# Performance work log

Hardware: AMD Instinct MI355X
Metric: run time of the kernel (lower is better)

The kernel has to match this reference:

```python
import jax, jax.numpy as jnp
import numpy as np

B, M, N = 4, 1024, 32768

def setup_inputs() -> dict:
    key = jax.random.key(0)
    k1, k2 = jax.random.split(key)
    keypoints = jax.random.normal(k1, (B, 3, M), dtype=jnp.float32)
    pc = jax.random.normal(k2, (B, 3, N), dtype=jnp.float32)
    return {"keypoints": keypoints, "pc": pc}

def reference(keypoints, pc):
    # Pairwise Euclidean distances via the expanded quadratic form:
    # ||k - p||^2 = ||k||^2 + ||p||^2 - 2 k.p  -> avoids the [B,3,M,N] tensor.
    k2 = jnp.sum(keypoints * keypoints, axis=1)            # [B, M]
    p2 = jnp.sum(pc * pc, axis=1)                          # [B, N]
    cross = jnp.einsum("bdm,bdn->bmn", keypoints, pc)     # [B, M, N]
    d2 = k2[:, :, None] + p2[:, None, :] - 2.0 * cross     # [B, M, N]
    dist = jnp.sqrt(jnp.maximum(d2, 0.0))
    min_dist = jnp.min(dist, axis=2)                       # [B, M]
    return jnp.mean(min_dist)
```

## Files before the change

### kernel.cpp

```cpp
#include <hip/hip_runtime.h>
#include <math.h>

#define BATCH 4
#define M 1024
#define NPTS 32768
#define NSPLIT 128
#define CHUNK (NPTS / NSPLIT)
#define KPT 4
#define TPB 256
#define RBLOCKS 16

#define Q_OFF      0
#define D2P_OFF    (2u << 20)
#define GSUM_OFF   (4u << 20)
#define CNT_OFF    ((4u << 20) + 4u)

__global__ __launch_bounds__(256) void p2p_prep(
        const float* __restrict__ pc, float4* __restrict__ q,
        float* __restrict__ gsum, unsigned* __restrict__ counter) {
    int i = blockIdx.x * 256 + threadIdx.x;
    int b = i >> 15;
    int n = i & (NPTS - 1);
    const float* p = pc + (size_t)b * 3 * NPTS;
    float x = p[n], y = p[NPTS + n], z = p[2 * NPTS + n];
    float hp = -0.5f * fmaf(x, x, fmaf(y, y, z * z));
    q[i] = make_float4(x, y, z, hp);
    if (i == 0) { *gsum = 0.f; *counter = 0u; }
}

__global__ __launch_bounds__(TPB) void p2p_main(
        const float* __restrict__ kp, const float4* __restrict__ q,
        float* __restrict__ d2p) {
    const int b = blockIdx.x / NSPLIT;
    const int c = blockIdx.x % NSPLIT;
    const int t = threadIdx.x;

    const float4* qc = q + b * NPTS + c * CHUNK;
    const float* kpb = kp + (size_t)b * 3 * M;

    float kx[KPT], ky[KPT], kz[KPT], k2[KPT], md[KPT];
#pragma unroll
    for (int k = 0; k < KPT; ++k) {
        int m = t + k * TPB;
        kx[k] = kpb[m];
        ky[k] = kpb[M + m];
        kz[k] = kpb[2 * M + m];
        k2[k] = fmaf(kx[k], kx[k], fmaf(ky[k], ky[k], kz[k] * kz[k]));
        md[k] = -INFINITY;
    }

#pragma unroll 2
    for (int j = 0; j < CHUNK; j += 4) {
        float4 q0 = qc[j + 0];
        float4 q1 = qc[j + 1];
        float4 q2 = qc[j + 2];
        float4 q3 = qc[j + 3];
#pragma unroll
        for (int k = 0; k < KPT; ++k) {
            float v0 = fmaf(kx[k], q0.x, fmaf(ky[k], q0.y, fmaf(kz[k], q0.z, q0.w)));
            float v1 = fmaf(kx[k], q1.x, fmaf(ky[k], q1.y, fmaf(kz[k], q1.z, q1.w)));
            float v2 = fmaf(kx[k], q2.x, fmaf(ky[k], q2.y, fmaf(kz[k], q2.z, q2.w)));
            float v3 = fmaf(kx[k], q3.x, fmaf(ky[k], q3.y, fmaf(kz[k], q3.z, q3.w)));
            md[k] = fmaxf(md[k], fmaxf(fmaxf(v0, v1), fmaxf(v2, v3)));
        }
    }

#pragma unroll
    for (int k = 0; k < KPT; ++k) {
        float d2 = fmaxf(fmaf(-2.f, md[k], k2[k]), 0.f);
        d2p[c * (BATCH * M) + b * M + t + k * TPB] = d2;
    }
}

__global__ __launch_bounds__(256) void p2p_reduce(
        const float* __restrict__ d2p, float* __restrict__ gsum,
        unsigned* __restrict__ counter, float* __restrict__ out) {
    const int i = blockIdx.x * 256 + threadIdx.x;
    float m0 = INFINITY, m1 = INFINITY;
#pragma unroll 4
    for (int c = 0; c < NSPLIT; c += 2) {
        m0 = fminf(m0, d2p[(c + 0) * (BATCH * M) + i]);
        m1 = fminf(m1, d2p[(c + 1) * (BATCH * M) + i]);
    }
    float s = sqrtf(fminf(m0, m1));
#pragma unroll
    for (int off = 32; off > 0; off >>= 1) s += __shfl_down(s, off, 64);
    __shared__ float sb[4];
    if ((threadIdx.x & 63) == 0) sb[threadIdx.x >> 6] = s;
    __syncthreads();
    if (threadIdx.x == 0) {
        float bsum = sb[0] + sb[1] + sb[2] + sb[3];
        atomicAdd(gsum, bsum);
        __threadfence();
        unsigned tk = atomicAdd(counter, 1u);
        if (tk == RBLOCKS - 1) {
            float total = atomicAdd(gsum, 0.0f);
            out[0] = total / (float)(BATCH * M);
        }
    }
}

extern "C" void kernel_launch(void* const* d_in, const int* in_sizes, int n_in,
                              void* d_out, int out_size, void* d_ws, size_t ws_size,
                              hipStream_t stream) {
    const float* kp = (const float*)d_in[0];
    const float* pc = (const float*)d_in[1];
    float* out = (float*)d_out;
    char* ws = (char*)d_ws;
    float4* q = (float4*)(ws + Q_OFF);
    float* d2p = (float*)(ws + D2P_OFF);
    float* gsum = (float*)(ws + GSUM_OFF);
    unsigned* counter = (unsigned*)(ws + CNT_OFF);

    p2p_prep<<<BATCH * NPTS / 256, 256, 0, stream>>>(pc, q, gsum, counter);
    p2p_main<<<BATCH * NSPLIT, TPB, 0, stream>>>(kp, q, d2p);
    p2p_reduce<<<RBLOCKS, 256, 0, stream>>>(d2p, gsum, counter, out);
}
```

Before: 83.29 us.

## Fuse point prep into main kernel, stage in LDS, use packed FMA

Removes the separate prep kernel: each main block loads its chunk of points into shared memory as SoA and computes the half-norm term itself, and also resets the reduction counters. The inner loop now uses v_pk_fma_f32 through inline asm to process two points per instruction. NSPLIT is doubled to 256 to launch more blocks, and the reduce kernel gets four accumulators. This drops one launch and a global round trip but doubles the partial-result traffic in the reduce step, and the counter reset now relies on block 0 of the main kernel running before the reduce kernel.

Measured after the change: 78.17 us. 1.07x faster.

```diff
diff --git a/kernel.cpp b/kernel.cpp
--- a/kernel.cpp
+++ b/kernel.cpp
@@ -4,64 +4,77 @@
 #define BATCH 4
 #define M 1024
 #define NPTS 32768
-#define NSPLIT 128
+#define NSPLIT 256
 #define CHUNK (NPTS / NSPLIT)
 #define KPT 4
 #define TPB 256
 #define RBLOCKS 16
 
-#define Q_OFF      0
-#define D2P_OFF    (2u << 20)
+#define D2P_OFF    0
 #define GSUM_OFF   (4u << 20)
 #define CNT_OFF    ((4u << 20) + 4u)
 
-__global__ __launch_bounds__(256) void p2p_prep(
-        const float* __restrict__ pc, float4* __restrict__ q,
-        float* __restrict__ gsum, unsigned* __restrict__ counter) {
-    int i = blockIdx.x * 256 + threadIdx.x;
-    int b = i >> 15;
-    int n = i & (NPTS - 1);
-    const float* p = pc + (size_t)b * 3 * NPTS;
-    float x = p[n], y = p[NPTS + n], z = p[2 * NPTS + n];
-    float hp = -0.5f * fmaf(x, x, fmaf(y, y, z * z));
-    q[i] = make_float4(x, y, z, hp);
-    if (i == 0) { *gsum = 0.f; *counter = 0u; }
+typedef float v2f __attribute__((ext_vector_type(2)));
+
+__device__ inline v2f pk_fma(v2f a, v2f b, v2f c) {
+    v2f d;
+    asm("v_pk_fma_f32 %0, %1, %2, %3" : "=v"(d) : "v"(a), "v"(b), "v"(c));
+    return d;
 }
 
 __global__ __launch_bounds__(TPB) void p2p_main(
-        const float* __restrict__ kp, const float4* __restrict__ q,
-        float* __restrict__ d2p) {
+        const float* __restrict__ kp, const float* __restrict__ pc,
+        float* __restrict__ d2p, float* __restrict__ gsum,
+        unsigned* __restrict__ counter) {
+    __shared__ __align__(16) float qx[CHUNK];
+    __shared__ __align__(16) float qy[CHUNK];
+    __shared__ __align__(16) float qz[CHUNK];
+    __shared__ __align__(16) float qh[CHUNK];
+
     const int b = blockIdx.x / NSPLIT;
     const int c = blockIdx.x % NSPLIT;
     const int t = threadIdx.x;
 
-    const float4* qc = q + b * NPTS + c * CHUNK;
+    if (blockIdx.x == 0 && t == 0) { *gsum = 0.f; *counter = 0u; }
+
+    const float* pcb = pc + (size_t)b * 3 * NPTS + c * CHUNK;
+    if (t < CHUNK) {
+        float x = pcb[t], y = pcb[NPTS + t], z = pcb[2 * NPTS + t];
+        qx[t] = x; qy[t] = y; qz[t] = z;
+        qh[t] = -0.5f * fmaf(x, x, fmaf(y, y, z * z));
+    }
+
     const float* kpb = kp + (size_t)b * 3 * M;
-
-    float kx[KPT], ky[KPT], kz[KPT], k2[KPT], md[KPT];
+    v2f kx2[KPT], ky2[KPT], kz2[KPT];
+    float k2[KPT], md[KPT];
 #pragma unroll
     for (int k = 0; k < KPT; ++k) {
         int m = t + k * TPB;
-        kx[k] = kpb[m];
-        ky[k] = kpb[M + m];
-        kz[k] = kpb[2 * M + m];
-        k2[k] = fmaf(kx[k], kx[k], fmaf(ky[k], ky[k], kz[k] * kz[k]));
+        float x = kpb[m], y = kpb[M + m], z = kpb[2 * M + m];
+        kx2[k] = (v2f){x, x};
+        ky2[k] = (v2f){y, y};
+        kz2[k] = (v2f){z, z};
+        k2[k] = fmaf(x, x, fmaf(y, y, z * z));
         md[k] = -INFINITY;
     }
+    __syncthreads();
 
-#pragma unroll 2
+#pragma unroll 4
     for (int j = 0; j < CHUNK; j += 4) {
-        float4 q0 = qc[j + 0];
-        float4 q1 = qc[j + 1];
-        float4 q2 = qc[j + 2];
-        float4 q3 = qc[j + 3];
+        float4 X = *(const float4*)&qx[j];
+        float4 Y = *(const float4*)&qy[j];
+        float4 Z = *(const float4*)&qz[j];
+        float4 H = *(const float4*)&qh[j];
+        v2f X01 = {X.x, X.y}, X23 = {X.z, X.w};
+        v2f Y01 = {Y.x, Y.y}, Y23 = {Y.z, Y.w};
+        v2f Z01 = {Z.x, Z.y}, Z23 = {Z.z, Z.w};
+        v2f H01 = {H.x, H.y}, H23 = {H.z, H.w};
 #pragma unroll
         for (int k = 0; k < KPT; ++k) {
-            float v0 = fmaf(kx[k], q0.x, fmaf(ky[k], q0.y, fmaf(kz[k], q0.z, q0.w)));
-            float v1 = fmaf(kx[k], q1.x, fmaf(ky[k], q1.y, fmaf(kz[k], q1.z, q1.w)));
-            float v2 = fmaf(kx[k], q2.x, fmaf(ky[k], q2.y, fmaf(kz[k], q2.z, q2.w)));
-            float v3 = fmaf(kx[k], q3.x, fmaf(ky[k], q3.y, fmaf(kz[k], q3.z, q3.w)));
-            md[k] = fmaxf(md[k], fmaxf(fmaxf(v0, v1), fmaxf(v2, v3)));
+            v2f u01 = pk_fma(kx2[k], X01, pk_fma(ky2[k], Y01, pk_fma(kz2[k], Z01, H01)));
+            v2f u23 = pk_fma(kx2[k], X23, pk_fma(ky2[k], Y23, pk_fma(kz2[k], Z23, H23)));
+            md[k] = fmaxf(fmaxf(md[k], u01.x), u01.y);
+            md[k] = fmaxf(fmaxf(md[k], u23.x), u23.y);
         }
     }
 
@@ -76,13 +89,15 @@
         const float* __restrict__ d2p, float* __restrict__ gsum,
         unsigned* __restrict__ counter, float* __restrict__ out) {
     const int i = blockIdx.x * 256 + threadIdx.x;
-    float m0 = INFINITY, m1 = INFINITY;
-#pragma unroll 4
-    for (int c = 0; c < NSPLIT; c += 2) {
+    float m0 = INFINITY, m1 = INFINITY, m2 = INFINITY, m3 = INFINITY;
+#pragma unroll 2
+    for (int c = 0; c < NSPLIT; c += 4) {
         m0 = fminf(m0, d2p[(c + 0) * (BATCH * M) + i]);
         m1 = fminf(m1, d2p[(c + 1) * (BATCH * M) + i]);
+        m2 = fminf(m2, d2p[(c + 2) * (BATCH * M) + i]);
+        m3 = fminf(m3, d2p[(c + 3) * (BATCH * M) + i]);
     }
-    float s = sqrtf(fminf(m0, m1));
+    float s = sqrtf(fminf(fminf(m0, m1), fminf(m2, m3)));
 #pragma unroll
     for (int off = 32; off > 0; off >>= 1) s += __shfl_down(s, off, 64);
     __shared__ float sb[4];
@@ -107,12 +122,10 @@
     const float* pc = (const float*)d_in[1];
     float* out = (float*)d_out;
     char* ws = (char*)d_ws;
-    float4* q = (float4*)(ws + Q_OFF);
     float* d2p = (float*)(ws + D2P_OFF);
     float* gsum = (float*)(ws + GSUM_OFF);
     unsigned* counter = (unsigned*)(ws + CNT_OFF);
 
-    p2p_prep<<<BATCH * NPTS / 256, 256, 0, stream>>>(pc, q, gsum, counter);
-    p2p_main<<<BATCH * NSPLIT, TPB, 0, stream>>>(kp, q, d2p);
+    p2p_main<<<BATCH * NSPLIT, TPB, 0, stream>>>(kp, pc, d2p, gsum, counter);
     p2p_reduce<<<RBLOCKS, 256, 0, stream>>>(d2p, gsum, counter, out);
 }
```
